# Optimization experiments

Measured on AMD Instinct MI355X. Metric: run time of the kernel, lower is better.

Reference implementation:

```python
import jax, jax.numpy as jnp
import numpy as np

N_NODES = 100000


def setup_inputs() -> dict:
    key = jax.random.key(0)
    k1, k2, k3, k4, k5 = jax.random.split(key, 5)
    features = jax.random.normal(k1, (N_NODES, 512), dtype=jnp.float32)
    src = jax.random.randint(k2, (1600000,), 0, N_NODES, dtype=jnp.int64)
    dst = jax.random.randint(k3, (1600000,), 0, N_NODES, dtype=jnp.int64)
    # Glorot-ish init for the two GraphConv weights (bias=False)
    W1 = jax.random.normal(k4, (512, 64), dtype=jnp.float32) / np.sqrt(512.0)
    W2 = jax.random.normal(k5, (64, 512), dtype=jnp.float32) / np.sqrt(64.0)
    return {"features": features, "src": src, "dst": dst, "W1": W1, "W2": W2}


def _graph_conv(x, W, src, dst, norm_src, norm_dst):
    """DGL GraphConv, norm='both', bias=False.
    Applies W before aggregation when in_feats > out_feats (as DGL does)."""
    weight_first = W.shape[0] > W.shape[1]
    if weight_first:
        x = x @ W  # [N, out]
    msgs = x[src] * norm_src[src, None]                  # gather + src norm
    agg = jax.ops.segment_sum(msgs, dst, num_segments=N_NODES)
    h = agg * norm_dst[:, None]                          # dst norm
    if not weight_first:
        h = h @ W
    return h


def reference(features, src, dst, W1, W2):
    ones = jnp.ones(src.shape[0], dtype=features.dtype)
    deg_out = jax.ops.segment_sum(ones, src, num_segments=N_NODES)
    deg_in = jax.ops.segment_sum(ones, dst, num_segments=N_NODES)
    norm_src = jnp.where(deg_out > 0, deg_out, 1.0) ** -0.5
    norm_dst = jnp.where(deg_in > 0, deg_in, 1.0) ** -0.5
    h = _graph_conv(features, W1, src, dst, norm_src, norm_dst)
    h = jax.nn.relu(h)
    # dropout is identity in eval mode
    x_hat = _graph_conv(h, W2, src, dst, norm_src, norm_dst)
    return x_hat
```

## Files before the change

kernel.cpp:

```cpp
#include <hip/hip_runtime.h>


__launch_bounds__(256)
__global__ void gemm1_hist_kernel(const float* __restrict__ A, const float* __restrict__ B,
                                  float* __restrict__ C, int M,
                                  const int* __restrict__ src, const int* __restrict__ dst,
                                  float* __restrict__ degO, int* __restrict__ cnt,
                                  int* __restrict__ rank, int E, int gemmBlocks) {
    __shared__ __align__(16) float As[32][132];
    __shared__ __align__(16) float Bs[32][64];

    if ((int)blockIdx.x >= gemmBlocks) {
        int hb = blockIdx.x - gemmBlocks;
        int histThreads = (gridDim.x - gemmBlocks) * 256;
        for (int e = hb * 256 + threadIdx.x; e < E; e += histThreads) {
            int s = src[e];
            int d = dst[e];
            atomicAdd(&degO[s], 1.0f);
            rank[e] = atomicAdd(&cnt[d], 1);
        }
        return;
    }

    const int tid = threadIdx.x;
    const int txn = tid & 7;
    const int tym = tid >> 3;
    const int rowBase = blockIdx.x * 128;

    float4 ra[4];
    float4 rb[2];

    auto gload = [&](int k0) {
#pragma unroll
        for (int p = 0; p < 4; ++p) {
            int idx = p * 256 + tid;
            int r  = idx >> 3;
            int kv = (idx & 7) * 4;
            int gr = rowBase + r;
            ra[p] = make_float4(0.f, 0.f, 0.f, 0.f);
            if (gr < M) ra[p] = *(const float4*)(A + (size_t)gr * 512 + k0 + kv);
        }
#pragma unroll
        for (int p = 0; p < 2; ++p) {
            int idx = p * 256 + tid;
            int kr = idx >> 4;
            int nv = (idx & 15) * 4;
            rb[p] = *(const float4*)(B + (size_t)(k0 + kr) * 64 + nv);
        }
    };

    float acc[4][8];
#pragma unroll
    for (int i = 0; i < 4; ++i)
#pragma unroll
        for (int j = 0; j < 8; ++j) acc[i][j] = 0.0f;

    gload(0);
    for (int k0 = 0; k0 < 512; k0 += 32) {
#pragma unroll
        for (int p = 0; p < 4; ++p) {
            int idx = p * 256 + tid;
            int r  = idx >> 3;
            int kv = (idx & 7) * 4;
            As[kv + 0][r] = ra[p].x; As[kv + 1][r] = ra[p].y;
            As[kv + 2][r] = ra[p].z; As[kv + 3][r] = ra[p].w;
        }
#pragma unroll
        for (int p = 0; p < 2; ++p) {
            int idx = p * 256 + tid;
            int kr = idx >> 4;
            int nv = (idx & 15) * 4;
            *(float4*)&Bs[kr][nv] = rb[p];
        }
        __syncthreads();
        if (k0 + 32 < 512) gload(k0 + 32);

#pragma unroll 8
        for (int k = 0; k < 32; ++k) {
            float a[4], b[8];
            *(float4*)&a[0] = *(const float4*)&As[k][tym * 4];
            *(float4*)&b[0] = *(const float4*)&Bs[k][txn * 8];
            *(float4*)&b[4] = *(const float4*)&Bs[k][txn * 8 + 4];
#pragma unroll
            for (int i = 0; i < 4; ++i)
#pragma unroll
                for (int j = 0; j < 8; ++j)
                    acc[i][j] = fmaf(a[i], b[j], acc[i][j]);
        }
        __syncthreads();
    }

#pragma unroll
    for (int i = 0; i < 4; ++i) {
        int gr = rowBase + tym * 4 + i;
        if (gr < M) {
            *(float4*)(C + (size_t)gr * 64 + txn * 8) =
                make_float4(acc[i][0], acc[i][1], acc[i][2], acc[i][3]);
            *(float4*)(C + (size_t)gr * 64 + txn * 8 + 4) =
                make_float4(acc[i][4], acc[i][5], acc[i][6], acc[i][7]);
        }
    }
}

__global__ void scan_pass1(const int* __restrict__ cnt, int* __restrict__ rowptr,
                           int* __restrict__ bsum, int n) {
    __shared__ int tmp[256];
    int tid = threadIdx.x;
    int i = blockIdx.x * 256 + tid;
    int v = (i < n) ? cnt[i] : 0;
    tmp[tid] = v;
    __syncthreads();
    for (int off = 1; off < 256; off <<= 1) {
        int t = (tid >= off) ? tmp[tid - off] : 0;
        __syncthreads();
        tmp[tid] += t;
        __syncthreads();
    }
    if (i < n) rowptr[i] = tmp[tid] - v;
    if (tid == 255) bsum[blockIdx.x] = tmp[255];
}

__global__ void scan_pass2(int* __restrict__ bsum, int nb) {
    __shared__ int tmp[512];
    int tid = threadIdx.x;
    int v = (tid < nb) ? bsum[tid] : 0;
    tmp[tid] = v;
    __syncthreads();
    for (int off = 1; off < 512; off <<= 1) {
        int t = (tid >= off) ? tmp[tid - off] : 0;
        __syncthreads();
        tmp[tid] += t;
        __syncthreads();
    }
    if (tid < nb) bsum[tid] = tmp[tid] - v;
}

__global__ void scan3_norm(int* __restrict__ rowptr, const int* __restrict__ bsum,
                           float* __restrict__ ns, float* __restrict__ nd,
                           float* __restrict__ scale2, const int* __restrict__ cnt,
                           int n, int E) {
    int i = blockIdx.x * 256 + threadIdx.x;
    if (i < n) {
        rowptr[i] += bsum[blockIdx.x];
        float a = rsqrtf(fmaxf(ns[i], 1.0f));
        float b = rsqrtf(fmaxf((float)cnt[i], 1.0f));
        ns[i] = a; nd[i] = b; scale2[i] = a * b;
    }
    if (i == 0) rowptr[n] = E;
}

__global__ void fill_csr(const int* __restrict__ src, const int* __restrict__ dst,
                         const int* __restrict__ rank, const int* __restrict__ rowptr,
                         int* __restrict__ csr, int E) {
    int e = blockIdx.x * blockDim.x + threadIdx.x;
    if (e < E) {
        csr[rowptr[dst[e]] + rank[e]] = src[e];
    }
}

template <bool RELU>
__global__ void gather_kernel(const float* __restrict__ x, const int* __restrict__ rowptr,
                              const int* __restrict__ csr, const float* __restrict__ scale,
                              float* __restrict__ out, int N) {
    int node = blockIdx.x * 4 + (threadIdx.x >> 6);
    if (node >= N) return;
    int lane = threadIdx.x & 63;
    int beg = rowptr[node], end = rowptr[node + 1];
    float acc = 0.0f;
    int i = beg;
    for (; i + 1 < end; i += 2) {
        int s0 = csr[i], s1 = csr[i + 1];
        float sc0 = scale[s0], sc1 = scale[s1];
        float v0 = x[(size_t)s0 * 64 + lane];
        float v1 = x[(size_t)s1 * 64 + lane];
        if (RELU) { v0 = fmaxf(v0, 0.0f); v1 = fmaxf(v1, 0.0f); }
        acc = fmaf(v0, sc0, acc);
        acc = fmaf(v1, sc1, acc);
    }
    if (i < end) {
        int s = csr[i];
        float v = x[(size_t)s * 64 + lane];
        if (RELU) v = fmaxf(v, 0.0f);
        acc = fmaf(v, scale[s], acc);
    }
    out[(size_t)node * 64 + lane] = acc;
}

__launch_bounds__(256)
__global__ void gemm2_kernel(const float* __restrict__ A, const float* __restrict__ nd,
                             const float* __restrict__ B, float* __restrict__ C, int M) {
    __shared__ __align__(16) float As[64][132];
    __shared__ __align__(16) float Bs[64][132];
    const int tid = threadIdx.x;
    const int txn = tid & 15;
    const int tym = tid >> 4;
    const int rowBase = blockIdx.x * 128;
    const int colBase = blockIdx.y * 128;

#pragma unroll
    for (int p = 0; p < 8; ++p) {
        int idx = p * 256 + tid;
        int r  = idx >> 4;
        int kv = (idx & 15) * 4;
        int gr = rowBase + r;
        float4 v = make_float4(0.f, 0.f, 0.f, 0.f);
        if (gr < M) {
            v = *(const float4*)(A + (size_t)gr * 64 + kv);
            float s = nd[gr];
            v.x *= s; v.y *= s; v.z *= s; v.w *= s;
        }
        As[kv + 0][r] = v.x; As[kv + 1][r] = v.y;
        As[kv + 2][r] = v.z; As[kv + 3][r] = v.w;
    }
#pragma unroll
    for (int p = 0; p < 8; ++p) {
        int idx = p * 256 + tid;
        int kr = idx >> 5;
        int nv = (idx & 31) * 4;
        *(float4*)&Bs[kr][nv] = *(const float4*)(B + (size_t)kr * 512 + colBase + nv);
    }
    __syncthreads();

    float acc[8][8];
#pragma unroll
    for (int i = 0; i < 8; ++i)
#pragma unroll
        for (int j = 0; j < 8; ++j) acc[i][j] = 0.0f;

#pragma unroll 4
    for (int k = 0; k < 64; ++k) {
        float a[8], b[8];
        *(float4*)&a[0] = *(const float4*)&As[k][tym * 8];
        *(float4*)&a[4] = *(const float4*)&As[k][tym * 8 + 4];
        *(float4*)&b[0] = *(const float4*)&Bs[k][txn * 4];
        *(float4*)&b[4] = *(const float4*)&Bs[k][64 + txn * 4];
#pragma unroll
        for (int i = 0; i < 8; ++i)
#pragma unroll
            for (int j = 0; j < 8; ++j)
                acc[i][j] = fmaf(a[i], b[j], acc[i][j]);
    }

#pragma unroll
    for (int i = 0; i < 8; ++i) {
        int gr = rowBase + tym * 8 + i;
        if (gr < M) {
            *(float4*)(C + (size_t)gr * 512 + colBase + txn * 4) =
                make_float4(acc[i][0], acc[i][1], acc[i][2], acc[i][3]);
            *(float4*)(C + (size_t)gr * 512 + colBase + 64 + txn * 4) =
                make_float4(acc[i][4], acc[i][5], acc[i][6], acc[i][7]);
        }
    }
}

extern "C" void kernel_launch(void* const* d_in, const int* in_sizes, int n_in,
                              void* d_out, int out_size, void* d_ws, size_t ws_size,
                              hipStream_t stream) {
    const float* feat = (const float*)d_in[0];
    const int*   src  = (const int*)d_in[1];
    const int*   dst  = (const int*)d_in[2];
    const float* W1   = (const float*)d_in[3];
    const float* W2   = (const float*)d_in[4];
    const int N = in_sizes[0] / 512;
    const int E = in_sizes[1];
    float* out = (float*)d_out;

    float* ns     = (float*)d_ws;
    float* nd     = ns + N;
    float* scale2 = nd + N;
    int*   cnt    = (int*)(scale2 + N);
    int*   rowptr = cnt + N;
    int*   bsum   = rowptr + (N + 1);
    int*   csr    = bsum + 512;
    float* buf1   = (float*)(((unsigned long long)(csr + E) + 15ull) & ~15ull);
    float* agg1   = buf1 + (size_t)64 * N;
    int*   rank   = (int*)agg1;

    hipMemsetAsync(ns, 0, (size_t)N * sizeof(float), stream);
    hipMemsetAsync(cnt, 0, (size_t)N * sizeof(int), stream);

    const int gemmBlocks = (N + 127) / 128;
    const int histBlocks = 512;
    gemm1_hist_kernel<<<gemmBlocks + histBlocks, 256, 0, stream>>>(
        feat, W1, buf1, N, src, dst, ns, cnt, rank, E, gemmBlocks);

    const int nb = (N + 255) / 256;
    scan_pass1<<<nb, 256, 0, stream>>>(cnt, rowptr, bsum, N);
    scan_pass2<<<1, 512, 0, stream>>>(bsum, nb);
    scan3_norm<<<nb, 256, 0, stream>>>(rowptr, bsum, ns, nd, scale2, cnt, N, E);

    fill_csr<<<(E + 255) / 256, 256, 0, stream>>>(src, dst, rank, rowptr, csr, E);

    gather_kernel<false><<<(N + 3) / 4, 256, 0, stream>>>(buf1, rowptr, csr, ns, agg1, N);

    gather_kernel<true><<<(N + 3) / 4, 256, 0, stream>>>(agg1, rowptr, csr, scale2, buf1, N);

    gemm2_kernel<<<dim3((N + 127) / 128, 4), 256, 0, stream>>>(buf1, nd, W2, out, N);
}
```

Measured before the change: 751.6 us.

## Fuse second-layer gather aggregation into GEMM2 via shared-memory tile

Merges the second sparse gather (ReLU, source scaling, destination norm) into the final GEMM kernel. Each block aggregates 64 destination rows into shared memory, then loops over all four 128-column tiles of W2 to write the output. This removes the intermediate 64-wide buffer write and re-read plus one kernel launch. In exchange, each block runs the irregular gather serially before any compute, with fewer blocks overall and a smaller per-thread GEMM tile.

```diff
diff --git a/kernel.cpp b/kernel.cpp
--- a/kernel.cpp
+++ b/kernel.cpp
@@ -187,69 +187,87 @@
 }
 
 __launch_bounds__(256)
-__global__ void gemm2_kernel(const float* __restrict__ A, const float* __restrict__ nd,
-                             const float* __restrict__ B, float* __restrict__ C, int M) {
-    __shared__ __align__(16) float As[64][132];
+__global__ void gather_gemm2_kernel(const float* __restrict__ agg1,
+                                    const int* __restrict__ rowptr,
+                                    const int* __restrict__ csr,
+                                    const float* __restrict__ scale2,
+                                    const float* __restrict__ nd,
+                                    const float* __restrict__ B,
+                                    float* __restrict__ C, int N) {
+    __shared__ __align__(16) float As[64][68];
     __shared__ __align__(16) float Bs[64][132];
-    const int tid = threadIdx.x;
+    const int tid  = threadIdx.x;
+    const int lane = tid & 63;
+    const int wave = tid >> 6;
+    const int rowBase = blockIdx.x * 64;
+
+    for (int j = 0; j < 16; ++j) {
+        int rloc = wave * 16 + j;
+        int gr = rowBase + rloc;
+        float acc = 0.0f;
+        if (gr < N) {
+            int beg = rowptr[gr], end = rowptr[gr + 1];
+            int i = beg;
+            for (; i + 1 < end; i += 2) {
+                int s0 = csr[i], s1 = csr[i + 1];
+                float v0 = fmaxf(agg1[(size_t)s0 * 64 + lane], 0.0f);
+                float v1 = fmaxf(agg1[(size_t)s1 * 64 + lane], 0.0f);
+                acc = fmaf(v0, scale2[s0], acc);
+                acc = fmaf(v1, scale2[s1], acc);
+            }
+            if (i < end) {
+                int s = csr[i];
+                acc = fmaf(fmaxf(agg1[(size_t)s * 64 + lane], 0.0f), scale2[s], acc);
+            }
+            acc *= nd[gr];
+        }
+        As[lane][rloc] = acc;
+    }
+    __syncthreads();
+
     const int txn = tid & 15;
     const int tym = tid >> 4;
-    const int rowBase = blockIdx.x * 128;
-    const int colBase = blockIdx.y * 128;
-
-#pragma unroll
-    for (int p = 0; p < 8; ++p) {
-        int idx = p * 256 + tid;
-        int r  = idx >> 4;
-        int kv = (idx & 15) * 4;
-        int gr = rowBase + r;
-        float4 v = make_float4(0.f, 0.f, 0.f, 0.f);
-        if (gr < M) {
-            v = *(const float4*)(A + (size_t)gr * 64 + kv);
-            float s = nd[gr];
-            v.x *= s; v.y *= s; v.z *= s; v.w *= s;
-        }
-        As[kv + 0][r] = v.x; As[kv + 1][r] = v.y;
-        As[kv + 2][r] = v.z; As[kv + 3][r] = v.w;
-    }
-#pragma unroll
-    for (int p = 0; p < 8; ++p) {
-        int idx = p * 256 + tid;
-        int kr = idx >> 5;
-        int nv = (idx & 31) * 4;
-        *(float4*)&Bs[kr][nv] = *(const float4*)(B + (size_t)kr * 512 + colBase + nv);
-    }
-    __syncthreads();
-
-    float acc[8][8];
-#pragma unroll
-    for (int i = 0; i < 8; ++i)
-#pragma unroll
-        for (int j = 0; j < 8; ++j) acc[i][j] = 0.0f;
+    for (int ct = 0; ct < 4; ++ct) {
+        const int colBase = ct * 128;
+#pragma unroll
+        for (int p = 0; p < 8; ++p) {
+            int idx = p * 256 + tid;
+            int kr = idx >> 5;
+            int nv = (idx & 31) * 4;
+            *(float4*)&Bs[kr][nv] = *(const float4*)(B + (size_t)kr * 512 + colBase + nv);
+        }
+        __syncthreads();
+
+        float acc2[4][8];
+#pragma unroll
+        for (int i = 0; i < 4; ++i)
+#pragma unroll
+            for (int j = 0; j < 8; ++j) acc2[i][j] = 0.0f;
 
 #pragma unroll 4
-    for (int k = 0; k < 64; ++k) {
-        float a[8], b[8];
-        *(float4*)&a[0] = *(const float4*)&As[k][tym * 8];
-        *(float4*)&a[4] = *(const float4*)&As[k][tym * 8 + 4];
-        *(float4*)&b[0] = *(const float4*)&Bs[k][txn * 4];
-        *(float4*)&b[4] = *(const float4*)&Bs[k][64 + txn * 4];
-#pragma unroll
-        for (int i = 0; i < 8; ++i)
-#pragma unroll
-            for (int j = 0; j < 8; ++j)
-                acc[i][j] = fmaf(a[i], b[j], acc[i][j]);
-    }
-
-#pragma unroll
-    for (int i = 0; i < 8; ++i) {
-        int gr = rowBase + tym * 8 + i;
-        if (gr < M) {
-            *(float4*)(C + (size_t)gr * 512 + colBase + txn * 4) =
-                make_float4(acc[i][0], acc[i][1], acc[i][2], acc[i][3]);
-            *(float4*)(C + (size_t)gr * 512 + colBase + 64 + txn * 4) =
-                make_float4(acc[i][4], acc[i][5], acc[i][6], acc[i][7]);
-        }
+        for (int k = 0; k < 64; ++k) {
+            float a[4], b[8];
+            *(float4*)&a[0] = *(const float4*)&As[k][tym * 4];
+            *(float4*)&b[0] = *(const float4*)&Bs[k][txn * 4];
+            *(float4*)&b[4] = *(const float4*)&Bs[k][64 + txn * 4];
+#pragma unroll
+            for (int i = 0; i < 4; ++i)
+#pragma unroll
+                for (int j = 0; j < 8; ++j)
+                    acc2[i][j] = fmaf(a[i], b[j], acc2[i][j]);
+        }
+
+#pragma unroll
+        for (int i = 0; i < 4; ++i) {
+            int gr = rowBase + tym * 4 + i;
+            if (gr < N) {
+                *(float4*)(C + (size_t)gr * 512 + colBase + txn * 4) =
+                    make_float4(acc2[i][0], acc2[i][1], acc2[i][2], acc2[i][3]);
+                *(float4*)(C + (size_t)gr * 512 + colBase + 64 + txn * 4) =
+                    make_float4(acc2[i][4], acc2[i][5], acc2[i][6], acc2[i][7]);
+            }
+        }
+        __syncthreads();
     }
 }
 
@@ -293,7 +311,6 @@
 
     gather_kernel<false><<<(N + 3) / 4, 256, 0, stream>>>(buf1, rowptr, csr, ns, agg1, N);
 
-    gather_kernel<true><<<(N + 3) / 4, 256, 0, stream>>>(agg1, rowptr, csr, scale2, buf1, N);
-
-    gemm2_kernel<<<dim3((N + 127) / 128, 4), 256, 0, stream>>>(buf1, nd, W2, out, N);
-}
+    gather_gemm2_kernel<<<(N + 63) / 64, 256, 0, stream>>>(
+        agg1, rowptr, csr, scale2, nd, W2, out, N);
+}
```

New measurement: 902.8 us. +20.1%, slower.
